# Kernel optimization log

Measured on AMD Instinct MI355X. Metric: run time of the kernel, lower is better.

## Reference

```python
import jax, jax.numpy as jnp
import numpy as np
import math

B, S, D, H, FF = 2, 2048, 1024, 16, 4096
DH = D // H
EPS = 1e-5


def layernorm(x, g, b):
    mu = jnp.mean(x, axis=-1, keepdims=True)
    var = jnp.mean((x - mu) ** 2, axis=-1, keepdims=True)
    return (x - mu) * jax.lax.rsqrt(var + EPS) * g + b


def setup_inputs() -> dict:
    key = jax.random.key(0)
    ks = jax.random.split(key, 8)
    s = lambda fan_in: 1.0 / math.sqrt(fan_in)
    return {
        "x": jax.random.normal(ks[0], (B, S, D), jnp.float32),
        "attention_mask": jnp.zeros((B, 1, 1, S), jnp.float32),
        "wq": jax.random.uniform(ks[1], (D, D), jnp.float32, -s(D), s(D)),
        "wk": jax.random.uniform(ks[2], (D, D), jnp.float32, -s(D), s(D)),
        "wv": jax.random.uniform(ks[3], (D, D), jnp.float32, -s(D), s(D)),
        "wo": jax.random.uniform(ks[4], (D, D), jnp.float32, -s(D), s(D)),
        "w1": jax.random.uniform(ks[5], (D, FF), jnp.float32, -s(D), s(D)),
        "w2": jax.random.uniform(ks[6], (FF, D), jnp.float32, -s(FF), s(FF)),
        "ln1_g": jnp.ones((D,), jnp.float32),
        "ln1_b": jnp.zeros((D,), jnp.float32),
        "ln2_g": jnp.ones((D,), jnp.float32),
        "ln2_b": jnp.zeros((D,), jnp.float32),
    }


def reference(x, attention_mask, wq, wk, wv, wo, w1, w2, ln1_g, ln1_b, ln2_g, ln2_b):
    # --- attention ResNorm (pre-LN) ---
    y = layernorm(x, ln1_g, ln1_b)
    q = (y @ wq).reshape(B, S, H, DH)
    k = (y @ wk).reshape(B, S, H, DH)
    v = (y @ wv).reshape(B, S, H, DH)
    # NOTE: original scales by sqrt(hidden_dim), not sqrt(head_dim)
    scores = jnp.einsum("bqhd,bkhd->bhqk", q, k) / math.sqrt(D) + attention_mask
    probs = jax.nn.softmax(scores, axis=-1)
    attn = jnp.einsum("bhqk,bkhd->bqhd", probs, v).reshape(B, S, D)
    x = x + attn @ wo
    # --- FFN ResNorm ---
    y = layernorm(x, ln2_g, ln2_b)
    y = jax.nn.gelu(y @ w1, approximate=False) @ w2
    return x + y
```

## Files before the change

kernel.cpp:

```cpp
#include <hip/hip_runtime.h>
#include <hip/hip_bf16.h>
#include <math.h>

#define Bb 2
#define Ss 2048
#define Dd 1024
#define Hh 16
#define FFf 4096
#define EPSf 1e-5f
#define SCALEf 0.03125f
#define LOG2Ef 1.4426950408889634f
#define SCALE2f (SCALEf * LOG2Ef)
#define KSPLIT 4
#define NTILES ((Ss / KSPLIT) / 64)

typedef short s16x8 __attribute__((ext_vector_type(8)));
typedef short s16x4 __attribute__((ext_vector_type(4)));
typedef float f32x4 __attribute__((ext_vector_type(4)));
typedef float f32x16 __attribute__((ext_vector_type(16)));

__device__ __forceinline__ short f2bs(float f) {
    union { float f; unsigned u; } v; v.f = f;
    const unsigned r = (v.u + 0x7FFFu + ((v.u >> 16) & 1u)) >> 16;
    return (short)r;
}
__device__ __forceinline__ float bs2f(short s) {
    union { unsigned u; float f; } v; v.u = ((unsigned)(unsigned short)s) << 16;
    return v.f;
}
__device__ __forceinline__ float gelu_exact(float v) {
    return 0.5f * v * (1.0f + erff(v * 0.7071067811865475f));
}
__device__ __forceinline__ void gload16(const void* g, void* l) {
    __builtin_amdgcn_global_load_lds(
        (const __attribute__((address_space(1))) unsigned int*)g,
        (__attribute__((address_space(3))) unsigned int*)l, 16, 0, 0);
}
__device__ __forceinline__ unsigned cvt_pk(float lo, float hi) {
    unsigned r;
    asm("v_cvt_pk_bf16_f32 %0, %1, %2" : "=v"(r) : "v"(lo), "v"(hi));
    return r;
}

__global__ __launch_bounds__(256) void prep(const float* __restrict__ wq, const float* __restrict__ wk,
                                            const float* __restrict__ wv, const float* __restrict__ wo,
                                            const float* __restrict__ w1, const float* __restrict__ w2,
                                            const float* __restrict__ mask,
                                            short* __restrict__ qkvw_t, short* __restrict__ wot,
                                            short* __restrict__ w1t, short* __restrict__ w2t,
                                            float* __restrict__ msc) {
    const int blk = blockIdx.x;
    const int tid = threadIdx.x;
    if (blk >= 3072) {
#pragma unroll
        for (int j = 0; j < 16; ++j) msc[tid + j * 256] = mask[tid + j * 256] * LOG2Ef;
        return;
    }
    const float* W; short* Wt; int K, N, inner;
    if (blk < 1024) {
        const int which = blk >> 8; inner = blk & 255;
        K = 1024; N = 1024;
        W = (which == 0) ? wq : (which == 1) ? wk : (which == 2) ? wv : wo;
        Wt = (which < 3) ? qkvw_t + (size_t)which * 1024 * 1024 : wot;
    } else if (blk < 2048) {
        inner = blk - 1024; K = 1024; N = 4096; W = w1; Wt = w1t;
    } else {
        inner = blk - 2048; K = 4096; N = 1024; W = w2; Wt = w2t;
    }
    const int nbx = N / 64;
    const int bx = inner % nbx, by = inner / nbx;
    __shared__ short T[64][65];
    const int n0 = bx * 64, k0 = by * 64;
    const int c = tid & 63, rg = tid >> 6;
#pragma unroll
    for (int j = 0; j < 16; ++j) {
        const int r = rg * 16 + j;
        T[r][c] = f2bs(W[(size_t)(k0 + r) * N + n0 + c]);
    }
    __syncthreads();
#pragma unroll
    for (int j = 0; j < 16; ++j) {
        const int r = rg * 16 + j;
        Wt[(size_t)(n0 + r) * K + k0 + c] = T[c][r];
    }
}

__global__ __launch_bounds__(256) void vtranspose(const short* __restrict__ QKV,
                                                  short* __restrict__ VT) {
    __shared__ __align__(16) short T[64 * 144];
    const int t = threadIdx.x;
    const int bh = blockIdx.x;
    const int sc = blockIdx.y;
    const int b = bh >> 4, h = bh & 15;
#pragma unroll
    for (int i = 0; i < 4; ++i) {
        const int sl = i * 32 + (t >> 3);
        const int d0 = (t & 7) * 8;
        const s16x8 v = *(const s16x8*)&QKV[((size_t)(b * Ss + sc * 128 + sl)) * 3072 + 2048 + h * 64 + d0];
#pragma unroll
        for (int e = 0; e < 8; ++e) {
            const int d = d0 + e;
            T[(d * 144 + sl) ^ (((d >> 3) & 7) << 3)] = v[e];
        }
    }
    __syncthreads();
#pragma unroll
    for (int i = 0; i < 4; ++i) {
        const int d = i * 16 + (t >> 4);
        const int s0 = (t & 15) * 8;
        const s16x8 o = *(const s16x8*)&T[(d * 144 + s0) ^ (((d >> 3) & 7) << 3)];
        *(s16x8*)&VT[((size_t)(bh * 64 + d)) * 2048 + sc * 128 + s0] = o;
    }
}

__global__ __launch_bounds__(256) void layernorm_bf16(const float* __restrict__ X,
                                                      const float* __restrict__ g,
                                                      const float* __restrict__ bta,
                                                      short* __restrict__ Y) {
    __shared__ float red[8];
    const int row = blockIdx.x;
    const int tid = threadIdx.x;
    const size_t base = (size_t)row * Dd + tid * 4;
    const float4 xv = *(const float4*)&X[base];
    float s  = xv.x + xv.y + xv.z + xv.w;
    float sq = xv.x * xv.x + xv.y * xv.y + xv.z * xv.z + xv.w * xv.w;
#pragma unroll
    for (int o = 32; o >= 1; o >>= 1) {
        s  += __shfl_xor(s, o, 64);
        sq += __shfl_xor(sq, o, 64);
    }
    const int lane = tid & 63, wv = tid >> 6;
    if (lane == 0) { red[wv] = s; red[4 + wv] = sq; }
    __syncthreads();
    const float tot  = red[0] + red[1] + red[2] + red[3];
    const float totq = red[4] + red[5] + red[6] + red[7];
    const float mu  = tot * (1.0f / Dd);
    const float var = totq * (1.0f / Dd) - mu * mu;
    const float inv = 1.0f / sqrtf(var + EPSf);
    const float4 gv = *(const float4*)&g[tid * 4];
    const float4 bv = *(const float4*)&bta[tid * 4];
    s16x4 o;
    o[0] = f2bs((xv.x - mu) * inv * gv.x + bv.x);
    o[1] = f2bs((xv.y - mu) * inv * gv.y + bv.y);
    o[2] = f2bs((xv.z - mu) * inv * gv.z + bv.z);
    o[3] = f2bs((xv.w - mu) * inv * gv.w + bv.w);
    *(s16x4*)&Y[base] = o;
}

template <int BM, int BN, int EPI>
__global__ __launch_bounds__(256) void gemm_v2(const short* __restrict__ A,
                                               const short* __restrict__ Bt,
                                               const float* __restrict__ R,
                                               void* __restrict__ Cout,
                                               int M, int N, int K) {
    constexpr int WM = BM / 2, WN = BN / 2;
    constexpr int MF = WM / 16, NF = WN / 16;
    __shared__ __align__(16) short As[2][BM * 64];
    __shared__ __align__(16) short Bs[2][BN * 64];

    const int tid = threadIdx.x;
    const int w = tid >> 6, l = tid & 63;
    const int lr = l & 15, lg = l >> 4;
    const int wr = w >> 1, wc = w & 1;
    const int bx = blockIdx.x, by = blockIdx.y;

    const int srp   = l >> 3;
    const int sslot = ((l & 7) ^ (srp & 7)) * 8;
    const size_t arow0 = (size_t)(by * BM);
    const size_t brow0 = (size_t)(bx * BN);

    f32x4 acc[NF][MF] = {};

    auto STAGE = [&](int bi, int k0) {
#pragma unroll
        for (int j = 0; j < BM / 32; ++j) {
            const int r0 = w * (BM / 4) + j * 8;
            gload16(A + (arow0 + r0 + srp) * K + k0 + sslot, &As[bi][r0 * 64]);
        }
#pragma unroll
        for (int j = 0; j < BN / 32; ++j) {
            const int r0 = w * (BN / 4) + j * 8;
            gload16(Bt + (brow0 + r0 + srp) * K + k0 + sslot, &Bs[bi][r0 * 64]);
        }
    };

    STAGE(0, 0);
    int cur = 0;

    for (int k0 = 0; k0 < K; k0 += 64) {
        asm volatile("s_waitcnt vmcnt(0)" ::: "memory");
        __builtin_amdgcn_s_barrier();
        if (k0 + 64 < K) STAGE(cur ^ 1, k0 + 64);

#pragma unroll
        for (int kk = 0; kk < 2; ++kk) {
            s16x8 a[MF], b[NF];
#pragma unroll
            for (int m = 0; m < MF; ++m) {
                const int r = wr * WM + m * 16 + lr;
                a[m] = *(const s16x8*)&As[cur][r * 64 + (((kk * 4 + lg) ^ (r & 7)) * 8)];
            }
#pragma unroll
            for (int n = 0; n < NF; ++n) {
                const int r = wc * WN + n * 16 + lr;
                b[n] = *(const s16x8*)&Bs[cur][r * 64 + (((kk * 4 + lg) ^ (r & 7)) * 8)];
            }
#pragma unroll
            for (int n = 0; n < NF; ++n)
#pragma unroll
                for (int m = 0; m < MF; ++m)
                    acc[n][m] = __builtin_amdgcn_mfma_f32_16x16x32_bf16(b[n], a[m], acc[n][m], 0, 0, 0);
        }
        cur ^= 1;
    }

    const int row0 = by * BM + wr * WM;
    const int col0 = bx * BN + wc * WN;
#pragma unroll
    for (int m = 0; m < MF; ++m) {
        const int row = row0 + m * 16 + lr;
#pragma unroll
        for (int n = 0; n < NF; ++n) {
            const int cb = col0 + n * 16 + lg * 4;
            if (EPI == 2) {
                float* C = (float*)Cout;
                const f32x4 r4 = *(const f32x4*)&R[(size_t)row * N + cb];
                f32x4 o;
#pragma unroll
                for (int r = 0; r < 4; ++r) o[r] = acc[n][m][r] + r4[r];
                *(f32x4*)&C[(size_t)row * N + cb] = o;
            } else {
                s16x4 o;
#pragma unroll
                for (int r = 0; r < 4; ++r) {
                    float v = acc[n][m][r];
                    if (EPI == 1) v = gelu_exact(v);
                    o[r] = f2bs(v);
                }
                *(s16x4*)&((short*)Cout)[(size_t)row * N + cb] = o;
            }
        }
    }
}

__global__ __launch_bounds__(256) void attn_split(const short* __restrict__ QKV,
                                                  const short* __restrict__ VT,
                                                  const float* __restrict__ MSC,
                                                  short* __restrict__ Opart,
                                                  float2* __restrict__ ML) {
    __shared__ __align__(16) short Kbuf[2][64 * 64];
    __shared__ __align__(16) short Vbuf[2][64 * 64];

    const int tid = threadIdx.x;
    const int w = tid >> 6, l = tid & 63;
    const int col = l & 31;
    const int hi = l >> 5;

    const int bid = blockIdx.x;
    const int part = bid >> 9;
    const int inner = bid & 511;
    const int qt = inner & 15, h = (inner >> 4) & 15, b = inner >> 8;
    const int q0 = qt * 128 + w * 32;
    const int k_base = part * (Ss / KSPLIT);

    s16x8 qf[4];
    {
        const short* qsrc = QKV + ((size_t)(b * Ss + q0 + col)) * 3072 + h * 64 + hi * 8;
        qf[0] = *(const s16x8*)(qsrc);
        qf[1] = *(const s16x8*)(qsrc + 16);
        qf[2] = *(const s16x8*)(qsrc + 32);
        qf[3] = *(const s16x8*)(qsrc + 48);
    }

    const int sr   = l >> 3;
    const int slot = ((l & 7) ^ (sr & 7)) * 8;
    const short* kg = QKV + (size_t)(b * Ss) * 3072 + 1024 + h * 64 + (size_t)sr * 3072 + slot;
    const short* vg = VT + ((size_t)(b * Hh + h) * 64 + sr) * 2048 + k_base + slot;
    const float* mscb = MSC + (size_t)b * Ss + k_base;

    f32x16 o_acc[2] = {};
    float m_used = -1e30f, l_run = 0.0f;

    auto STAGE = [&](int bi, int t) {
#pragma unroll
        for (int j = 0; j < 2; ++j) {
            const int r0 = w * 16 + j * 8;
            gload16(kg + (size_t)(k_base + t * 64 + r0) * 3072, &Kbuf[bi][r0 * 64]);
            gload16(vg + (size_t)r0 * 2048 + t * 64,             &Vbuf[bi][r0 * 64]);
        }
    };

    STAGE(0, 0);
    int cur = 0;

    for (int i = 0; i < NTILES; ++i) {
        asm volatile("s_waitcnt vmcnt(0)" ::: "memory");
        __builtin_amdgcn_s_barrier();
        if (i + 1 < NTILES) STAGE(cur ^ 1, i + 1);

#pragma unroll
        for (int sub = 0; sub < 2; ++sub) {
            f32x16 sa = {};
            const int rk = sub * 32 + col;
#pragma unroll
            for (int dd = 0; dd < 4; ++dd) {
                const s16x8 kf = *(const s16x8*)&Kbuf[cur][rk * 64 + ((2 * dd + hi) ^ (rk & 7)) * 8];
                sa = __builtin_amdgcn_mfma_f32_32x32x16_bf16(kf, qf[dd], sa, 0, 0, 0);
            }

#pragma unroll
            for (int c4 = 0; c4 < 4; ++c4) {
                const f32x4 mv = *(const f32x4*)&mscb[i * 64 + sub * 32 + 8 * c4 + 4 * hi];
#pragma unroll
                for (int rr = 0; rr < 4; ++rr) sa[c4 * 4 + rr] = sa[c4 * 4 + rr] * SCALE2f + mv[rr];
            }
            float t8[8], t4[4];
#pragma unroll
            for (int r = 0; r < 8; ++r) t8[r] = fmaxf(sa[2 * r], sa[2 * r + 1]);
#pragma unroll
            for (int r = 0; r < 4; ++r) t4[r] = fmaxf(t8[2 * r], t8[2 * r + 1]);
            float tmax = fmaxf(fmaxf(t4[0], t4[1]), fmaxf(t4[2], t4[3]));
            {
                unsigned a = __float_as_uint(tmax), bq = __float_as_uint(tmax);
                asm volatile("v_permlane32_swap_b32 %0, %1" : "+v"(a), "+v"(bq));
                tmax = fmaxf(tmax, __uint_as_float(hi ? a : bq));
            }
            if (__any(tmax > m_used + 8.0f)) {
                const float nm = fmaxf(m_used, tmax);
                const float corr = __builtin_amdgcn_exp2f(m_used - nm);
                m_used = nm;
                l_run *= corr;
#pragma unroll
                for (int dt = 0; dt < 2; ++dt)
#pragma unroll
                    for (int r = 0; r < 16; ++r) o_acc[dt][r] *= corr;
            }

            unsigned wd[8];
            float s8[8];
#pragma unroll
            for (int m8 = 0; m8 < 8; ++m8) {
                const float p0 = __builtin_amdgcn_exp2f(sa[2 * m8]     - m_used);
                const float p1 = __builtin_amdgcn_exp2f(sa[2 * m8 + 1] - m_used);
                s8[m8] = p0 + p1;
                wd[m8] = cvt_pk(p0, p1);
            }
            float s4[4];
#pragma unroll
            for (int r = 0; r < 4; ++r) s4[r] = s8[2 * r] + s8[2 * r + 1];
            l_run += (s4[0] + s4[1]) + (s4[2] + s4[3]);

            unsigned f00 = wd[0], f02 = wd[2];
            asm volatile("v_permlane32_swap_b32 %0, %1" : "+v"(f00), "+v"(f02));
            unsigned f01 = wd[1], f03 = wd[3];
            asm volatile("v_permlane32_swap_b32 %0, %1" : "+v"(f01), "+v"(f03));
            unsigned f10 = wd[4], f12 = wd[6];
            asm volatile("v_permlane32_swap_b32 %0, %1" : "+v"(f10), "+v"(f12));
            unsigned f11 = wd[5], f13 = wd[7];
            asm volatile("v_permlane32_swap_b32 %0, %1" : "+v"(f11), "+v"(f13));
            union { unsigned u[4]; s16x8 v; } pf0, pf1;
            pf0.u[0] = f00; pf0.u[1] = f01; pf0.u[2] = f02; pf0.u[3] = f03;
            pf1.u[0] = f10; pf1.u[1] = f11; pf1.u[2] = f12; pf1.u[3] = f13;

#pragma unroll
            for (int dt = 0; dt < 2; ++dt) {
                const int rv = dt * 32 + col;
                const s16x8 v0 = *(const s16x8*)&Vbuf[cur][rv * 64 + ((sub * 4 + 0 + hi) ^ (rv & 7)) * 8];
                const s16x8 v1 = *(const s16x8*)&Vbuf[cur][rv * 64 + ((sub * 4 + 2 + hi) ^ (rv & 7)) * 8];
                o_acc[dt] = __builtin_amdgcn_mfma_f32_32x32x16_bf16(v0, pf0.v, o_acc[dt], 0, 0, 0);
                o_acc[dt] = __builtin_amdgcn_mfma_f32_32x32x16_bf16(v1, pf1.v, o_acc[dt], 0, 0, 0);
            }
        }
        cur ^= 1;
    }

    float l_tot;
    {
        unsigned a = __float_as_uint(l_run), bq = __float_as_uint(l_run);
        asm volatile("v_permlane32_swap_b32 %0, %1" : "+v"(a), "+v"(bq));
        l_tot = l_run + __uint_as_float(hi ? a : bq);
    }
    const size_t tok = (size_t)(b * Ss + q0 + col);
    if (hi == 0) {
        ML[(size_t)part * (Bb * Ss * Hh) + tok * Hh + h] = make_float2(m_used, l_tot);
    }
    short* obase = Opart + (size_t)part * (Bb * Ss) * Dd + tok * Dd + h * 64;
#pragma unroll
    for (int dt = 0; dt < 2; ++dt) {
#pragma unroll
        for (int c4 = 0; c4 < 4; ++c4) {
            s16x4 ov;
#pragma unroll
            for (int rr = 0; rr < 4; ++rr) ov[rr] = f2bs(o_acc[dt][c4 * 4 + rr]);
            *(s16x4*)&obase[dt * 32 + 8 * c4 + 4 * hi] = ov;
        }
    }
}

__global__ __launch_bounds__(256) void attn_combine(const short* __restrict__ Opart,
                                                    const float2* __restrict__ ML,
                                                    short* __restrict__ Oa) {
    const int tok = blockIdx.x;
    const int t = threadIdx.x;
    const int h = t >> 4;
    const int d = (t & 15) * 4;
    float2 ml[KSPLIT];
    float M = -1e30f;
#pragma unroll
    for (int p = 0; p < KSPLIT; ++p) {
        ml[p] = ML[(size_t)p * (Bb * Ss * Hh) + (size_t)tok * Hh + h];
        M = fmaxf(M, ml[p].x);
    }
    float a[KSPLIT], denom = 0.0f;
#pragma unroll
    for (int p = 0; p < KSPLIT; ++p) {
        a[p] = __builtin_amdgcn_exp2f(ml[p].x - M);
        denom += ml[p].y * a[p];
    }
    const float inv = 1.0f / denom;
    const size_t off = (size_t)tok * Dd + h * 64 + d;
    float acc[4] = {};
#pragma unroll
    for (int p = 0; p < KSPLIT; ++p) {
        const s16x4 o4 = *(const s16x4*)&Opart[(size_t)p * (Bb * Ss) * Dd + off];
#pragma unroll
        for (int r = 0; r < 4; ++r) acc[r] += bs2f(o4[r]) * a[p];
    }
    s16x4 o;
#pragma unroll
    for (int r = 0; r < 4; ++r) o[r] = f2bs(acc[r] * inv);
    *(s16x4*)&Oa[off] = o;
}

extern "C" void kernel_launch(void* const* d_in, const int* in_sizes, int n_in,
                              void* d_out, int out_size, void* d_ws, size_t ws_size,
                              hipStream_t stream) {
    const float* x    = (const float*)d_in[0];
    const float* mask = (const float*)d_in[1];
    const float* wq   = (const float*)d_in[2];
    const float* wk   = (const float*)d_in[3];
    const float* wv   = (const float*)d_in[4];
    const float* wo   = (const float*)d_in[5];
    const float* w1   = (const float*)d_in[6];
    const float* w2   = (const float*)d_in[7];
    const float* ln1g = (const float*)d_in[8];
    const float* ln1b = (const float*)d_in[9];
    const float* ln2g = (const float*)d_in[10];
    const float* ln2b = (const float*)d_in[11];
    float* out = (float*)d_out;

    char* p = (char*)d_ws;
    short* qkvw_t = (short*)p; p += (size_t)3072 * 1024 * 2;
    short* wot    = (short*)p; p += (size_t)1024 * 1024 * 2;
    short* w1t    = (short*)p; p += (size_t)4096 * 1024 * 2;
    short* w2t    = (short*)p; p += (size_t)1024 * 4096 * 2;
    short* y_bf   = (short*)p; p += (size_t)4096 * 1024 * 2;
    short* qkv    = (short*)p; p += (size_t)4096 * 3072 * 2;
    short* attn_b = (short*)p; p += (size_t)4096 * 1024 * 2;
    short* y2_bf  = (short*)p; p += (size_t)4096 * 1024 * 2;
    char*  hregion = p;        p += (size_t)4096 * 4096 * 2;
    float* msc    = (float*)p; p += (size_t)Bb * Ss * 4;

    short*  h_bf   = (short*)hregion;
    short*  o_part = (short*)hregion;
    short*  vt     = y_bf;
    float2* ml     = (float2*)qkvw_t;

    const int M = Bb * Ss;

    prep<<<3073, 256, 0, stream>>>(wq, wk, wv, wo, w1, w2, mask, qkvw_t, wot, w1t, w2t, msc);
    layernorm_bf16<<<M, 256, 0, stream>>>(x, ln1g, ln1b, y_bf);
    gemm_v2<128, 128, 0><<<dim3(24, 32), 256, 0, stream>>>(y_bf, qkvw_t, nullptr, qkv, M, 3072, 1024);
    vtranspose<<<dim3(32, 16), 256, 0, stream>>>(qkv, vt);
    attn_split<<<KSPLIT * 512, 256, 0, stream>>>(qkv, vt, msc, o_part, ml);
    attn_combine<<<M, 256, 0, stream>>>(o_part, ml, attn_b);
    gemm_v2<64, 128, 2><<<dim3(8, 64), 256, 0, stream>>>(attn_b, wot, x, out, M, 1024, 1024);
    layernorm_bf16<<<M, 256, 0, stream>>>(out, ln2g, ln2b, y2_bf);
    gemm_v2<128, 128, 1><<<dim3(32, 32), 256, 0, stream>>>(y2_bf, w1t, nullptr, h_bf, M, 4096, 1024);
    gemm_v2<64, 128, 2><<<dim3(8, 64), 256, 0, stream>>>(h_bf, w2t, out, out, M, 1024, 4096);
}
```

Before: 284.4 us.

## Triple-buffer GEMM k-loop with partial vmcnt waits and XCD-aware block swizzle

Replaces the double-buffered GEMM with a three-stage LDS pipeline. Two tiles are prefetched ahead, and each step waits only for the oldest outstanding loads rather than draining vmcnt to zero. It also makes the K-tile size a template parameter (32 for the 128x128 GEMMs) and launches a 1D grid remapped so consecutive blocks interleave across the 8 XCDs. The goals are to hide global-load latency, raise occupancy via launch_bounds(256,2), and improve L2 locality. In exchange it uses more LDS per block, and the hand-coded vmcnt counts must match the number of loads issued per stage.

```diff
diff --git a/kernel.cpp b/kernel.cpp
--- a/kernel.cpp
+++ b/kernel.cpp
@@ -147,25 +147,35 @@
     *(s16x4*)&Y[base] = o;
 }
 
-template <int BM, int BN, int EPI>
-__global__ __launch_bounds__(256) void gemm_v2(const short* __restrict__ A,
-                                               const short* __restrict__ Bt,
-                                               const float* __restrict__ R,
-                                               void* __restrict__ Cout,
-                                               int M, int N, int K) {
+template <int BM, int BN, int BK, int EPI>
+__global__ __launch_bounds__(256, 2) void gemm_v3(const short* __restrict__ A,
+                                                  const short* __restrict__ Bt,
+                                                  const float* __restrict__ R,
+                                                  void* __restrict__ Cout,
+                                                  int M, int N, int K, int gx) {
     constexpr int WM = BM / 2, WN = BN / 2;
     constexpr int MF = WM / 16, NF = WN / 16;
-    __shared__ __align__(16) short As[2][BM * 64];
-    __shared__ __align__(16) short Bs[2][BN * 64];
+    constexpr int S   = BK / 8;
+    constexpr int LPR = BK / 8;
+    constexpr int RPI = 64 / LPR;
+    constexpr int IPWA = (BM / 4) / RPI;
+    constexpr int IPWB = (BN / 4) / RPI;
+    constexpr int IPW = IPWA + IPWB;
+    __shared__ __align__(16) short As[3][BM * BK];
+    __shared__ __align__(16) short Bs[3][BN * BK];
 
     const int tid = threadIdx.x;
     const int w = tid >> 6, l = tid & 63;
     const int lr = l & 15, lg = l >> 4;
     const int wr = w >> 1, wc = w & 1;
-    const int bx = blockIdx.x, by = blockIdx.y;
-
-    const int srp   = l >> 3;
-    const int sslot = ((l & 7) ^ (srp & 7)) * 8;
+
+    const int nwg = gridDim.x;
+    const int bid = blockIdx.x;
+    const int swz = (bid & 7) * (nwg >> 3) + (bid >> 3);
+    const int bx = swz % gx, by = swz / gx;
+
+    const int lrow = l / LPR;
+    const int sslot = ((l % LPR) ^ ((lrow * (BK / 64)) & (S - 1))) * 8;
     const size_t arow0 = (size_t)(by * BM);
     const size_t brow0 = (size_t)(bx * BN);
 
@@ -173,37 +183,49 @@
 
     auto STAGE = [&](int bi, int k0) {
 #pragma unroll
-        for (int j = 0; j < BM / 32; ++j) {
-            const int r0 = w * (BM / 4) + j * 8;
-            gload16(A + (arow0 + r0 + srp) * K + k0 + sslot, &As[bi][r0 * 64]);
-        }
-#pragma unroll
-        for (int j = 0; j < BN / 32; ++j) {
-            const int r0 = w * (BN / 4) + j * 8;
-            gload16(Bt + (brow0 + r0 + srp) * K + k0 + sslot, &Bs[bi][r0 * 64]);
+        for (int j = 0; j < IPWA; ++j) {
+            const int r0 = w * (BM / 4) + j * RPI;
+            gload16(A + (arow0 + r0 + lrow) * K + k0 + sslot, &As[bi][r0 * BK]);
+        }
+#pragma unroll
+        for (int j = 0; j < IPWB; ++j) {
+            const int r0 = w * (BN / 4) + j * RPI;
+            gload16(Bt + (brow0 + r0 + lrow) * K + k0 + sslot, &Bs[bi][r0 * BK]);
         }
     };
 
+    const int NKi = K / BK;
     STAGE(0, 0);
-    int cur = 0;
-
-    for (int k0 = 0; k0 < K; k0 += 64) {
-        asm volatile("s_waitcnt vmcnt(0)" ::: "memory");
+    STAGE(1, BK);
+
+    for (int ks = 0; ks < NKi; ++ks) {
+        const int cur = ks % 3;
+        if (ks + 1 < NKi) {
+            if constexpr (IPW == 4)      asm volatile("s_waitcnt vmcnt(4)" ::: "memory");
+            else if constexpr (IPW == 6) asm volatile("s_waitcnt vmcnt(6)" ::: "memory");
+            else if constexpr (IPW == 8) asm volatile("s_waitcnt vmcnt(8)" ::: "memory");
+            else                         asm volatile("s_waitcnt vmcnt(12)" ::: "memory");
+        } else {
+            asm volatile("s_waitcnt vmcnt(0)" ::: "memory");
+        }
+        __builtin_amdgcn_sched_barrier(0);
         __builtin_amdgcn_s_barrier();
-        if (k0 + 64 < K) STAGE(cur ^ 1, k0 + 64);
-
-#pragma unroll
-        for (int kk = 0; kk < 2; ++kk) {
+        if (ks + 2 < NKi) STAGE((ks + 2) % 3, (ks + 2) * BK);
+
+#pragma unroll
+        for (int kk = 0; kk < BK / 32; ++kk) {
             s16x8 a[MF], b[NF];
 #pragma unroll
             for (int m = 0; m < MF; ++m) {
                 const int r = wr * WM + m * 16 + lr;
-                a[m] = *(const s16x8*)&As[cur][r * 64 + (((kk * 4 + lg) ^ (r & 7)) * 8)];
+                const int q = (kk * 4 + lg) ^ ((r * (BK / 64)) & (S - 1));
+                a[m] = *(const s16x8*)&As[cur][r * BK + q * 8];
             }
 #pragma unroll
             for (int n = 0; n < NF; ++n) {
                 const int r = wc * WN + n * 16 + lr;
-                b[n] = *(const s16x8*)&Bs[cur][r * 64 + (((kk * 4 + lg) ^ (r & 7)) * 8)];
+                const int q = (kk * 4 + lg) ^ ((r * (BK / 64)) & (S - 1));
+                b[n] = *(const s16x8*)&Bs[cur][r * BK + q * 8];
             }
 #pragma unroll
             for (int n = 0; n < NF; ++n)
@@ -211,7 +233,6 @@
                 for (int m = 0; m < MF; ++m)
                     acc[n][m] = __builtin_amdgcn_mfma_f32_16x16x32_bf16(b[n], a[m], acc[n][m], 0, 0, 0);
         }
-        cur ^= 1;
     }
 
     const int row0 = by * BM + wr * WM;
@@ -470,12 +491,12 @@
 
     prep<<<3073, 256, 0, stream>>>(wq, wk, wv, wo, w1, w2, mask, qkvw_t, wot, w1t, w2t, msc);
     layernorm_bf16<<<M, 256, 0, stream>>>(x, ln1g, ln1b, y_bf);
-    gemm_v2<128, 128, 0><<<dim3(24, 32), 256, 0, stream>>>(y_bf, qkvw_t, nullptr, qkv, M, 3072, 1024);
+    gemm_v3<128, 128, 32, 0><<<768, 256, 0, stream>>>(y_bf, qkvw_t, nullptr, qkv, M, 3072, 1024, 24);
     vtranspose<<<dim3(32, 16), 256, 0, stream>>>(qkv, vt);
     attn_split<<<KSPLIT * 512, 256, 0, stream>>>(qkv, vt, msc, o_part, ml);
     attn_combine<<<M, 256, 0, stream>>>(o_part, ml, attn_b);
-    gemm_v2<64, 128, 2><<<dim3(8, 64), 256, 0, stream>>>(attn_b, wot, x, out, M, 1024, 1024);
+    gemm_v3<64, 128, 64, 2><<<512, 256, 0, stream>>>(attn_b, wot, x, out, M, 1024, 1024, 8);
     layernorm_bf16<<<M, 256, 0, stream>>>(out, ln2g, ln2b, y2_bf);
-    gemm_v2<128, 128, 1><<<dim3(32, 32), 256, 0, stream>>>(y2_bf, w1t, nullptr, h_bf, M, 4096, 1024);
-    gemm_v2<64, 128, 2><<<dim3(8, 64), 256, 0, stream>>>(h_bf, w2t, out, out, M, 1024, 4096);
-}
+    gemm_v3<128, 128, 32, 1><<<1024, 256, 0, stream>>>(y2_bf, w1t, nullptr, h_bf, M, 4096, 1024, 32);
+    gemm_v3<64, 128, 64, 2><<<512, 256, 0, stream>>>(h_bf, w2t, out, out, M, 1024, 4096, 8);
+}
```

Measured after the change: 285.5 us. Within noise of the previous version (+0.4%).
